# Optimization experiments

Hardware: AMD Instinct MI355X
Metric: run time of the kernel (lower is better)

The kernel has to match this reference:

```python
import jax, jax.numpy as jnp
import numpy as np

N2, N1, N0 = 25000, 50000, 100000
E2, E1, E0 = 250000, 500000, 1000000
CIN, H, COUT = 64, 128, 64
BN_EPS = 1e-5


def setup_inputs() -> dict:
    key = jax.random.key(0)
    ks = jax.random.split(key, 26)
    inp = {
        'x': jax.random.normal(ks[0], (N2, CIN), jnp.float32),
        'edge_index': jax.random.randint(ks[1], (2, E2), 0, N2),
        'xs0': jax.random.normal(ks[2], (N0, H), jnp.float32),
        'xs1': jax.random.normal(ks[3], (N1, H), jnp.float32),
        'ei0': jax.random.randint(ks[4], (2, E0), 0, N0),
        'ei1': jax.random.randint(ks[5], (2, E1), 0, N1),
        'ew0': jax.random.uniform(ks[6], (E0,), jnp.float32, 0.1, 1.0),
        'ew1': jax.random.uniform(ks[7], (E1,), jnp.float32, 0.1, 1.0),
        # pooling perms: unique indices of kept nodes at the finer level
        'perm0': jax.random.permutation(ks[8], N0)[:N1],
        'perm1': jax.random.permutation(ks[9], N1)[:N2],
        # GIN layer 1: in=64 -> hidden//2=64 (MLP: Lin, ReLU, Lin), then BN
        'W1a': 0.1 * jax.random.normal(ks[10], (CIN, H // 2), jnp.float32),
        'b1a': jnp.zeros((H // 2,), jnp.float32),
        'W1b': 0.1 * jax.random.normal(ks[11], (H // 2, H // 2), jnp.float32),
        'b1b': jnp.zeros((H // 2,), jnp.float32),
        'g1': jnp.ones((H // 2,), jnp.float32),
        'bt1': jnp.zeros((H // 2,), jnp.float32),
        # GIN layer 2: 64 -> hidden=128
        'W2a': 0.1 * jax.random.normal(ks[12], (H // 2, H), jnp.float32),
        'b2a': jnp.zeros((H,), jnp.float32),
        'W2b': 0.1 * jax.random.normal(ks[13], (H, H), jnp.float32),
        'b2b': jnp.zeros((H,), jnp.float32),
        'g2': jnp.ones((H,), jnp.float32),
        'bt2': jnp.zeros((H,), jnp.float32),
        # GCN up_convs (improved=True): hidden->hidden, hidden->out
        'Wg0': 0.1 * jax.random.normal(ks[14], (H, H), jnp.float32),
        'bg0': jnp.zeros((H,), jnp.float32),
        'Wg1': 0.1 * jax.random.normal(ks[15], (H, COUT), jnp.float32),
        'bg1': jnp.zeros((COUT,), jnp.float32),
    }
    return inp


def _gin_layer(x, ei, Wa, ba, Wb, bb, g, bt):
    """GINConv (eps=0) + ReLU + BatchNorm1d (training-mode stats)."""
    n = x.shape[0]
    agg = jax.ops.segment_sum(x[ei[0]], ei[1], num_segments=n)
    h = x + agg  # (1 + eps) * x + sum of neighbors, eps = 0
    h = jnp.maximum(h @ Wa + ba, 0.0) @ Wb + bb  # MLP: Lin-ReLU-Lin
    h = jnp.maximum(h, 0.0)  # F.relu on conv output
    mu = h.mean(axis=0)
    var = jnp.mean((h - mu) ** 2, axis=0)  # biased var (BatchNorm1d)
    return g * (h - mu) * jax.lax.rsqrt(var + BN_EPS) + bt


def _gcn_improved(x, ei, ew, W, b):
    """GCNConv(improved=True): self-loop weight 2, symmetric norm."""
    n = x.shape[0]
    h = x @ W
    deg = jax.ops.segment_sum(ew, ei[1], num_segments=n) + 2.0  # +2I self loops
    dis = jax.lax.rsqrt(deg)
    norm = dis[ei[0]] * ew * dis[ei[1]]
    out = jax.ops.segment_sum(norm[:, None] * h[ei[0]], ei[1], num_segments=n)
    out = out + (2.0 * dis * dis)[:, None] * h  # self-loop contribution
    return out + b


def reference(x, edge_index, xs0, xs1, ei0, ei1, ew0, ew1, perm0, perm1,
              W1a, b1a, W1b, b1b, g1, bt1,
              W2a, b2a, W2b, b2b, g2, bt2,
              Wg0, bg0, Wg1, bg1):
    # projection convs on the coarsest graph
    h = _gin_layer(x, edge_index, W1a, b1a, W1b, b1b, g1, bt1)
    h = _gin_layer(h, edge_index, W2a, b2a, W2b, b2b, g2, bt2)
    # upsample step 1 (i=0, j=1): scatter into level-1 graph, GCN, ReLU
    up = jnp.zeros_like(xs1).at[perm1].set(h)
    h = jnp.maximum(_gcn_improved(up, ei1, ew1, Wg0, bg0), 0.0)
    # upsample step 2 (i=1, j=0): scatter into level-0 graph, final GCN
    up = jnp.zeros_like(xs0).at[perm0].set(h)
    return _gcn_improved(up, ei0, ew0, Wg1, bg1)
```

## Files before the change

kernel.cpp:

```cpp
#include <hip/hip_runtime.h>
#include <hip/hip_fp16.h>
#include <type_traits>

#define NN2 25000
#define NN1 50000
#define NN0 100000
#define EE2 250000
#define EE1 500000
#define EE0 1000000
#define NTOTC 175000
#define ETOTC 1750000
#define NB 684
#define CHUNK 2048
#define NBLK 855
#define BN_EPS 1e-5f

static inline int cdiv(long a, long b) { return (int)((a + b - 1) / b); }

typedef _Float16 half8 __attribute__((ext_vector_type(8)));
typedef float f32x4 __attribute__((ext_vector_type(4)));

template <int K, int M, bool RELU, bool BNIN, bool BNOUT, typename OT>
__global__ __launch_bounds__(256) void mfma_gemm_kernel(
    const __half* __restrict__ in, const float* __restrict__ W,
    const float* __restrict__ bias,
    const float* __restrict__ sums, const float* __restrict__ sumsq,
    const float* __restrict__ g, const float* __restrict__ bt,
    float* __restrict__ osum, float* __restrict__ osq,
    OT* __restrict__ out, int n)
{
    constexpr int BM = 64;
    constexpr int LDA = K + 8;
    constexpr int NC = M / 16;
    __shared__ __align__(16) _Float16 Ah[BM * LDA];
    __shared__ __align__(16) _Float16 Wt[M * LDA];
    const int tid = threadIdx.x;
    const int r0 = blockIdx.x * BM;

    for (int idx = tid; idx < K * M; idx += 256) {
        int k = idx / M, m = idx % M;
        Wt[m * LDA + k] = (_Float16)W[idx];
    }
    for (int idx = tid; idx < BM * K; idx += 256) {
        int r = idx / K, k = idx % K;
        int gr = r0 + r;
        float v = (gr < n) ? __half2float(in[(long)gr * K + k]) : 0.f;
        if (BNIN) {
            float mu = sums[k] * (1.f / NN2);
            float rs = rsqrtf(sumsq[k] * (1.f / NN2) - mu * mu + BN_EPS);
            v = g[k] * rs * (v - mu) + bt[k];
        }
        Ah[r * LDA + k] = (_Float16)v;
    }
    __syncthreads();

    const int wid = tid >> 6, lane = tid & 63;
    const int rw = wid * 16;
    const int arow = rw + (lane & 15);
    const int koff = (lane >> 4) * 8;

    f32x4 acc[NC];
    #pragma unroll
    for (int c = 0; c < NC; ++c) acc[c] = f32x4{0.f, 0.f, 0.f, 0.f};
    #pragma unroll
    for (int k0 = 0; k0 < K; k0 += 32) {
        half8 a = *(const half8*)&Ah[arow * LDA + k0 + koff];
        #pragma unroll
        for (int c = 0; c < NC; ++c) {
            half8 b = *(const half8*)&Wt[(c * 16 + (lane & 15)) * LDA + k0 + koff];
            acc[c] = __builtin_amdgcn_mfma_f32_16x16x32_f16(a, b, acc[c], 0, 0, 0);
        }
    }

    float* bs = (float*)Ah;
    if (BNOUT) {
        __syncthreads();
        if (tid < 2 * M) bs[tid] = 0.f;
        __syncthreads();
    }
    const int drow = r0 + rw + 4 * (lane >> 4);
    #pragma unroll
    for (int c = 0; c < NC; ++c) {
        int col = c * 16 + (lane & 15);
        float bv = (bias != nullptr) ? bias[col] : 0.f;
        float sc = 0.f, qc = 0.f;
        #pragma unroll
        for (int j = 0; j < 4; ++j) {
            int r = drow + j;
            if (r < n) {
                float v = acc[c][j] + bv;
                if (RELU) v = fmaxf(v, 0.f);
                if constexpr (std::is_same<OT, __half>::value)
                    out[(long)r * M + col] = __float2half(v);
                else
                    out[(long)r * M + col] = v;
                if (BNOUT) { sc += v; qc += v * v; }
            }
        }
        if (BNOUT) { atomicAdd(&bs[col], sc); atomicAdd(&bs[M + col], qc); }
    }
    if (BNOUT) {
        __syncthreads();
        if (tid < M) { atomicAdd(&osum[tid], bs[tid]); atomicAdd(&osq[tid], bs[M + tid]); }
    }
}

template <int K, int M1, int M2, bool BNOUT>
__global__ __launch_bounds__(256) void mlp_gemm_kernel(
    const __half* __restrict__ in,
    const float* __restrict__ W1, const float* __restrict__ b1,
    const float* __restrict__ W2, const float* __restrict__ b2,
    float* __restrict__ osum, float* __restrict__ osq,
    __half* __restrict__ out, int n)
{
    constexpr int BM = 64;
    constexpr int LDA = K + 8;
    constexpr int LDM = M1 + 8;
    constexpr int NC1 = M1 / 16, NC2 = M2 / 16;
    __shared__ __align__(16) _Float16 Ah[BM * LDA];
    __shared__ __align__(16) _Float16 Wt1[M1 * LDA];
    __shared__ __align__(16) _Float16 Wt2[M2 * LDM];
    __shared__ __align__(16) _Float16 mid[BM * LDM];
    const int tid = threadIdx.x;
    const int r0 = blockIdx.x * BM;

    for (int idx = tid; idx < K * M1; idx += 256) {
        int k = idx / M1, m = idx % M1;
        Wt1[m * LDA + k] = (_Float16)W1[idx];
    }
    for (int idx = tid; idx < M1 * M2; idx += 256) {
        int k = idx / M2, m = idx % M2;
        Wt2[m * LDM + k] = (_Float16)W2[idx];
    }
    for (int idx = tid; idx < BM * K; idx += 256) {
        int r = idx / K, k = idx % K;
        int gr = r0 + r;
        Ah[r * LDA + k] = (gr < n) ? (_Float16)in[(long)gr * K + k] : (_Float16)0.f;
    }
    __syncthreads();

    const int wid = tid >> 6, lane = tid & 63;
    const int rw = wid * 16;
    const int arow = rw + (lane & 15);
    const int koff = (lane >> 4) * 8;

    f32x4 acc1[NC1];
    #pragma unroll
    for (int c = 0; c < NC1; ++c) acc1[c] = f32x4{0.f, 0.f, 0.f, 0.f};
    #pragma unroll
    for (int k0 = 0; k0 < K; k0 += 32) {
        half8 a = *(const half8*)&Ah[arow * LDA + k0 + koff];
        #pragma unroll
        for (int c = 0; c < NC1; ++c) {
            half8 b = *(const half8*)&Wt1[(c * 16 + (lane & 15)) * LDA + k0 + koff];
            acc1[c] = __builtin_amdgcn_mfma_f32_16x16x32_f16(a, b, acc1[c], 0, 0, 0);
        }
    }
    {
        int rd0 = rw + 4 * (lane >> 4);
        #pragma unroll
        for (int c = 0; c < NC1; ++c) {
            int col = c * 16 + (lane & 15);
            float bv = b1[col];
            #pragma unroll
            for (int j = 0; j < 4; ++j)
                mid[(rd0 + j) * LDM + col] = (_Float16)fmaxf(acc1[c][j] + bv, 0.f);
        }
    }
    float* bs = (float*)Ah;
    if (BNOUT) {
        if (tid < 2 * M2) bs[tid] = 0.f;
    }
    __syncthreads();

    f32x4 acc2[NC2];
    #pragma unroll
    for (int c = 0; c < NC2; ++c) acc2[c] = f32x4{0.f, 0.f, 0.f, 0.f};
    #pragma unroll
    for (int k0 = 0; k0 < M1; k0 += 32) {
        half8 a = *(const half8*)&mid[arow * LDM + k0 + koff];
        #pragma unroll
        for (int c = 0; c < NC2; ++c) {
            half8 b = *(const half8*)&Wt2[(c * 16 + (lane & 15)) * LDM + k0 + koff];
            acc2[c] = __builtin_amdgcn_mfma_f32_16x16x32_f16(a, b, acc2[c], 0, 0, 0);
        }
    }
    const int drow = r0 + rw + 4 * (lane >> 4);
    #pragma unroll
    for (int c = 0; c < NC2; ++c) {
        int col = c * 16 + (lane & 15);
        float bv = b2[col];
        float sc = 0.f, qc = 0.f;
        #pragma unroll
        for (int j = 0; j < 4; ++j) {
            int r = drow + j;
            if (r < n) {
                float v = fmaxf(acc2[c][j] + bv, 0.f);
                out[(long)r * M2 + col] = __float2half(v);
                if (BNOUT) { sc += v; qc += v * v; }
            }
        }
        if (BNOUT) { atomicAdd(&bs[col], sc); atomicAdd(&bs[M2 + col], qc); }
    }
    if (BNOUT) {
        __syncthreads();
        if (tid < M2) { atomicAdd(&osum[tid], bs[tid]); atomicAdd(&osq[tid], bs[M2 + tid]); }
    }
}

__global__ void inv_tohalf_kernel(const int* __restrict__ perm1, const int* __restrict__ perm0,
                                  int* __restrict__ inv1, int* __restrict__ inv0,
                                  float* __restrict__ bnz,
                                  const float* __restrict__ x, __half* __restrict__ xh)
{
    int i = blockIdx.x * blockDim.x + threadIdx.x;
    if (i < 384) bnz[i] = 0.f;
    if (i < NN2) inv1[perm1[i]] = i;
    else if (i < NN2 + NN1) inv0[perm0[i - NN2]] = i - NN2;
    if (i < NN2 * 16) {
        float4 v = ((const float4*)x)[i];
        __half2 a = __floats2half2_rn(v.x, v.y);
        __half2 b = __floats2half2_rn(v.z, v.w);
        ((uint2*)xh)[i] = make_uint2(*(unsigned*)&a, *(unsigned*)&b);
    }
}

__global__ __launch_bounds__(256) void count_translate_kernel(
    const int* __restrict__ dst2,
    const int* __restrict__ src1, const int* __restrict__ dst1,
    const int* __restrict__ src0, const int* __restrict__ dst0,
    const int* __restrict__ inv1, const int* __restrict__ inv0,
    int* __restrict__ tcg, int* __restrict__ G)
{
    __shared__ int h[NB];
    int tid = threadIdx.x, blk = blockIdx.x;
    for (int i = tid; i < NB; i += 256) h[i] = 0;
    __syncthreads();
    int e0 = blk * CHUNK, e1 = min(e0 + CHUNK, ETOTC);
    for (int e = e0 + tid; e < e1; e += 256) {
        int vg;
        if (e < EE2) {
            vg = dst2[e];
        } else if (e < EE2 + EE1) {
            int i = e - EE2;
            vg = NN2 + dst1[i];
            tcg[i] = inv1[src1[i]];
        } else {
            int i = e - EE2 - EE1;
            vg = NN2 + NN1 + dst0[i];
            tcg[EE1 + i] = inv0[src0[i]];
        }
        atomicAdd(&h[vg >> 8], 1);
    }
    __syncthreads();
    for (int i = tid; i < NB; i += 256) G[i * NBLK + blk] = h[i];
}

__global__ __launch_bounds__(256) void scan_block_kernel(int* data, int* bsum, int n)
{
    __shared__ int sh[256];
    int tid = threadIdx.x;
    int base = blockIdx.x * 1024 + tid * 4;
    int v[4];
    #pragma unroll
    for (int i = 0; i < 4; ++i) v[i] = (base + i < n) ? data[base + i] : 0;
    int tot = v[0] + v[1] + v[2] + v[3];
    sh[tid] = tot;
    __syncthreads();
    for (int d = 1; d < 256; d <<= 1) {
        int add = (tid >= d) ? sh[tid - d] : 0;
        __syncthreads();
        sh[tid] += add;
        __syncthreads();
    }
    int run = sh[tid] - tot;
    #pragma unroll
    for (int i = 0; i < 4; ++i) {
        if (base + i < n) data[base + i] = run;
        run += v[i];
    }
    if (tid == 255) bsum[blockIdx.x] = sh[255];
}

__global__ __launch_bounds__(1024) void scan_bsum_kernel(int* bsum, int nb)
{
    __shared__ int sh[1024];
    int tid = threadIdx.x;
    int v = (tid < nb) ? bsum[tid] : 0;
    sh[tid] = v;
    __syncthreads();
    for (int d = 1; d < 1024; d <<= 1) {
        int add = (tid >= d) ? sh[tid - d] : 0;
        __syncthreads();
        sh[tid] += add;
        __syncthreads();
    }
    if (tid < nb) bsum[tid] = sh[tid] - v;
}

__global__ __launch_bounds__(256) void place_kernel(
    const int* __restrict__ src2, const int* __restrict__ dst2,
    const int* __restrict__ dst1, const float* __restrict__ ew1,
    const int* __restrict__ dst0, const float* __restrict__ ew0,
    const int* __restrict__ tcg,
    const int* __restrict__ G, const int* __restrict__ bsum,
    int2* __restrict__ bedges)
{
    __shared__ int cur[NB];
    int tid = threadIdx.x, blk = blockIdx.x;
    for (int i = tid; i < NB; i += 256) {
        int idx = i * NBLK + blk;
        cur[i] = G[idx] + bsum[idx >> 10];
    }
    __syncthreads();
    int e0 = blk * CHUNK, e1 = min(e0 + CHUNK, ETOTC);
    for (int e = e0 + tid; e < e1; e += 256) {
        int vg, c, ewb;
        if (e < EE2) {
            vg = dst2[e]; c = src2[e]; ewb = 0;
        } else if (e < EE2 + EE1) {
            int i = e - EE2;
            vg = NN2 + dst1[i]; c = tcg[i]; ewb = __float_as_int(ew1[i]);
        } else {
            int i = e - EE2 - EE1;
            vg = NN2 + NN1 + dst0[i]; c = tcg[EE1 + i]; ewb = __float_as_int(ew0[i]);
        }
        int b = vg >> 8, local = vg & 255;
        int pos = atomicAdd(&cur[b], 1);
        bedges[pos] = make_int2((local << 16) | (c + 1), ewb);
    }
}

__global__ __launch_bounds__(256) void bucket_build_kernel(
    const int2* __restrict__ bedges, const int* __restrict__ G,
    const int* __restrict__ bsum,
    int* __restrict__ rp, int* __restrict__ re,
    int2* __restrict__ csr, float* __restrict__ dis)
{
    __shared__ int cnt[256];
    __shared__ float wdeg[256];
    __shared__ int excl[256];
    __shared__ int tsum[256];
    int b = blockIdx.x, tid = threadIdx.x;
    int i0 = b * NBLK;
    int s0 = G[i0] + bsum[i0 >> 10];
    int s1;
    if (b == NB - 1) s1 = ETOTC;
    else { int i1 = (b + 1) * NBLK; s1 = G[i1] + bsum[i1 >> 10]; }
    cnt[tid] = 0; wdeg[tid] = 0.f;
    __syncthreads();
    for (int i = s0 + tid; i < s1; i += 256) {
        int2 t = bedges[i];
        int local = t.x >> 16;
        atomicAdd(&wdeg[local], __int_as_float(t.y));
        if (t.x & 0xFFFF) atomicAdd(&cnt[local], 1);
    }
    __syncthreads();
    int v = cnt[tid];
    tsum[tid] = v;
    __syncthreads();
    for (int d = 1; d < 256; d <<= 1) {
        int add = (tid >= d) ? tsum[tid - d] : 0;
        __syncthreads();
        tsum[tid] += add;
        __syncthreads();
    }
    excl[tid] = tsum[tid] - v;
    {
        int vg = (b << 8) + tid;
        if (vg < NTOTC) {
            int r0_ = s0 + excl[tid];
            rp[vg] = r0_;
            re[vg] = r0_ + v;
            if (vg >= NN2) dis[vg - NN2] = rsqrtf(wdeg[tid] + 2.0f);
        }
    }
    cnt[tid] = 0;
    __syncthreads();
    for (int i = s0 + tid; i < s1; i += 256) {
        int2 t = bedges[i];
        int cx = t.x & 0xFFFF;
        if (cx) {
            int local = t.x >> 16;
            int pos = s0 + excl[local] + atomicAdd(&cnt[local], 1);
            csr[pos] = make_int2(cx - 1, t.y);
        }
    }
}

__global__ void disc_kernel(const int* __restrict__ perm1, const int* __restrict__ perm0,
                            const float* __restrict__ dis,
                            float* __restrict__ disc1, float* __restrict__ disc0)
{
    int i = blockIdx.x * blockDim.x + threadIdx.x;
    if (i < NN2) disc1[i] = dis[perm1[i]];
    else if (i < NN2 + NN1) disc0[i - NN2] = dis[NN1 + perm0[i - NN2]];
}

template <bool BN>
__global__ __launch_bounds__(256) void gin_gather_kernel(
    const __half* __restrict__ x, const int* __restrict__ rp, const int* __restrict__ re,
    const int2* __restrict__ csr,
    const float* __restrict__ sums, const float* __restrict__ sumsq,
    const float* __restrict__ g, const float* __restrict__ bt,
    __half* __restrict__ out, int n)
{
    int v = (blockIdx.x * 256 + threadIdx.x) >> 5;
    int lane = threadIdx.x & 31;
    if (v >= n) return;
    int p0 = rp[v], pe = re[v];
    float2 sv = __half22float2(*(const __half2*)(x + (long)v * 64 + lane * 2));
    float ax[8], ay[8];
    #pragma unroll
    for (int u = 0; u < 8; ++u) { ax[u] = 0.f; ay[u] = 0.f; }
    ax[0] = sv.x; ay[0] = sv.y;
    for (int base = p0; base < pe; base += 32) {
        int idx = base + lane;
        int s_l = 0; float m_l = 0.f;
        if (idx < pe) { s_l = csr[idx].x; m_l = 1.f; }
        int cnt = min(32, pe - base);
        for (int j = 0; j < cnt; j += 8) {
            int ss[8]; float mm[8];
            #pragma unroll
            for (int u = 0; u < 8; ++u) {
                ss[u] = __shfl(s_l, j + u, 32);
                mm[u] = __shfl(m_l, j + u, 32);
            }
            float2 hh[8];
            #pragma unroll
            for (int u = 0; u < 8; ++u)
                hh[u] = __half22float2(*(const __half2*)(x + (long)ss[u] * 64 + lane * 2));
            #pragma unroll
            for (int u = 0; u < 8; ++u) {
                ax[u] = fmaf(mm[u], hh[u].x, ax[u]);
                ay[u] = fmaf(mm[u], hh[u].y, ay[u]);
            }
        }
    }
    float accx = ((ax[0] + ax[1]) + (ax[2] + ax[3])) + ((ax[4] + ax[5]) + (ax[6] + ax[7]));
    float accy = ((ay[0] + ay[1]) + (ay[2] + ay[3])) + ((ay[4] + ay[5]) + (ay[6] + ay[7]));
    if (BN) {
        int deg = pe - p0;
        int c0 = lane * 2, c1 = lane * 2 + 1;
        float mu0 = sums[c0] * (1.f / NN2), mu1 = sums[c1] * (1.f / NN2);
        float rs0 = rsqrtf(sumsq[c0] * (1.f / NN2) - mu0 * mu0 + BN_EPS);
        float rs1 = rsqrtf(sumsq[c1] * (1.f / NN2) - mu1 * mu1 + BN_EPS);
        float a0 = g[c0] * rs0, a1 = g[c1] * rs1;
        accx = a0 * accx + (float)(deg + 1) * (bt[c0] - a0 * mu0);
        accy = a1 * accy + (float)(deg + 1) * (bt[c1] - a1 * mu1);
    }
    *(__half2*)(out + (long)v * 64 + lane * 2) = __floats2half2_rn(accx, accy);
}

template <bool RELU>
__global__ __launch_bounds__(256) void gcn_gather128_kernel(
    const __half* __restrict__ cmp, const int* __restrict__ inv,
    const int* __restrict__ rp, const int* __restrict__ re,
    const int2* __restrict__ csr, const float* __restrict__ disc,
    const float* __restrict__ dis, const float* __restrict__ bias,
    __half* __restrict__ out, int n)
{
    int v = (blockIdx.x * 256 + threadIdx.x) >> 5;
    int lane = threadIdx.x & 31;
    if (v >= n) return;
    int p0 = rp[v], pe = re[v];
    f32x4 acc[8];
    #pragma unroll
    for (int u = 0; u < 8; ++u) acc[u] = f32x4{0.f, 0.f, 0.f, 0.f};
    for (int base = p0; base < pe; base += 32) {
        int idx = base + lane;
        int cs_l = 0; float w_l = 0.f;
        if (idx < pe) {
            int2 sl = csr[idx];
            cs_l = sl.x;
            w_l = __int_as_float(sl.y) * disc[sl.x];
        }
        int cnt = min(32, pe - base);
        for (int j = 0; j < cnt; j += 8) {
            int cc[8]; float ww[8];
            #pragma unroll
            for (int u = 0; u < 8; ++u) {
                cc[u] = __shfl(cs_l, j + u, 32);
                ww[u] = __shfl(w_l, j + u, 32);
            }
            uint2 uu[8];
            #pragma unroll
            for (int u = 0; u < 8; ++u)
                uu[u] = *(const uint2*)(cmp + (long)cc[u] * 128 + lane * 4);
            #pragma unroll
            for (int u = 0; u < 8; ++u) {
                float2 pa = __half22float2(*(__half2*)&uu[u].x);
                float2 pb = __half22float2(*(__half2*)&uu[u].y);
                acc[u][0] = fmaf(ww[u], pa.x, acc[u][0]);
                acc[u][1] = fmaf(ww[u], pa.y, acc[u][1]);
                acc[u][2] = fmaf(ww[u], pb.x, acc[u][2]);
                acc[u][3] = fmaf(ww[u], pb.y, acc[u][3]);
            }
        }
    }
    f32x4 tot = ((acc[0] + acc[1]) + (acc[2] + acc[3])) + ((acc[4] + acc[5]) + (acc[6] + acc[7]));
    float dv = dis[v];
    int cv = inv[v];
    float sx0 = 0.f, sx1 = 0.f, sx2 = 0.f, sx3 = 0.f;
    if (cv >= 0) {
        uint2 u = *(const uint2*)(cmp + (long)cv * 128 + lane * 4);
        float2 pa = __half22float2(*(__half2*)&u.x), pb = __half22float2(*(__half2*)&u.y);
        sx0 = pa.x; sx1 = pa.y; sx2 = pb.x; sx3 = pb.y;
    }
    float s2 = 2.f * dv * dv;
    float o0 = fmaf(dv, tot[0], fmaf(s2, sx0, bias[lane * 4]));
    float o1 = fmaf(dv, tot[1], fmaf(s2, sx1, bias[lane * 4 + 1]));
    float o2 = fmaf(dv, tot[2], fmaf(s2, sx2, bias[lane * 4 + 2]));
    float o3 = fmaf(dv, tot[3], fmaf(s2, sx3, bias[lane * 4 + 3]));
    if (RELU) {
        o0 = fmaxf(o0, 0.f); o1 = fmaxf(o1, 0.f);
        o2 = fmaxf(o2, 0.f); o3 = fmaxf(o3, 0.f);
    }
    __half2 ha = __floats2half2_rn(o0, o1), hb = __floats2half2_rn(o2, o3);
    *(uint2*)(out + (long)v * 128 + lane * 4) = make_uint2(*(unsigned*)&ha, *(unsigned*)&hb);
}

template <bool RELU>
__global__ __launch_bounds__(256) void gcn_gather64_kernel(
    const __half* __restrict__ cmp, const int* __restrict__ inv,
    const int* __restrict__ rp, const int* __restrict__ re,
    const int2* __restrict__ csr, const float* __restrict__ disc,
    const float* __restrict__ dis, const float* __restrict__ bias,
    float* __restrict__ out, int n)
{
    int v = (blockIdx.x * 256 + threadIdx.x) >> 5;
    int lane = threadIdx.x & 31;
    if (v >= n) return;
    int p0 = rp[v], pe = re[v];
    float ax[8], ay[8];
    #pragma unroll
    for (int u = 0; u < 8; ++u) { ax[u] = 0.f; ay[u] = 0.f; }
    for (int base = p0; base < pe; base += 32) {
        int idx = base + lane;
        int cs_l = 0; float w_l = 0.f;
        if (idx < pe) {
            int2 sl = csr[idx];
            cs_l = sl.x;
            w_l = __int_as_float(sl.y) * disc[sl.x];
        }
        int cnt = min(32, pe - base);
        for (int j = 0; j < cnt; j += 8) {
            int cc[8]; float ww[8];
            #pragma unroll
            for (int u = 0; u < 8; ++u) {
                cc[u] = __shfl(cs_l, j + u, 32);
                ww[u] = __shfl(w_l, j + u, 32);
            }
            float2 hh[8];
            #pragma unroll
            for (int u = 0; u < 8; ++u)
                hh[u] = __half22float2(*(const __half2*)(cmp + (long)cc[u] * 64 + lane * 2));
            #pragma unroll
            for (int u = 0; u < 8; ++u) {
                ax[u] = fmaf(ww[u], hh[u].x, ax[u]);
                ay[u] = fmaf(ww[u], hh[u].y, ay[u]);
            }
        }
    }
    float axs = ((ax[0] + ax[1]) + (ax[2] + ax[3])) + ((ax[4] + ax[5]) + (ax[6] + ax[7]));
    float ays = ((ay[0] + ay[1]) + (ay[2] + ay[3])) + ((ay[4] + ay[5]) + (ay[6] + ay[7]));
    float dv = dis[v];
    int cv = inv[v];
    float sx = 0.f, sy = 0.f;
    if (cv >= 0) {
        float2 hv = __half22float2(*(const __half2*)(cmp + (long)cv * 64 + lane * 2));
        sx = hv.x; sy = hv.y;
    }
    float s2 = 2.f * dv * dv;
    float o0 = fmaf(dv, axs, fmaf(s2, sx, bias[lane * 2]));
    float o1 = fmaf(dv, ays, fmaf(s2, sy, bias[lane * 2 + 1]));
    if (RELU) { o0 = fmaxf(o0, 0.f); o1 = fmaxf(o1, 0.f); }
    *(float2*)(out + (long)v * 64 + lane * 2) = make_float2(o0, o1);
}

extern "C" void kernel_launch(void* const* d_in, const int* in_sizes, int n_in,
                              void* d_out, int out_size, void* d_ws, size_t ws_size,
                              hipStream_t stream)
{
    const float* x    = (const float*)d_in[0];
    const int*   ei2  = (const int*)d_in[1];
    const int*   ei0  = (const int*)d_in[4];
    const int*   ei1  = (const int*)d_in[5];
    const float* ew0  = (const float*)d_in[6];
    const float* ew1  = (const float*)d_in[7];
    const int*   perm0= (const int*)d_in[8];
    const int*   perm1= (const int*)d_in[9];
    const float* W1a  = (const float*)d_in[10];
    const float* b1a  = (const float*)d_in[11];
    const float* W1b  = (const float*)d_in[12];
    const float* b1b  = (const float*)d_in[13];
    const float* g1   = (const float*)d_in[14];
    const float* bt1  = (const float*)d_in[15];
    const float* W2a  = (const float*)d_in[16];
    const float* b2a  = (const float*)d_in[17];
    const float* W2b  = (const float*)d_in[18];
    const float* b2b  = (const float*)d_in[19];
    const float* g2   = (const float*)d_in[20];
    const float* bt2  = (const float*)d_in[21];
    const float* Wg0  = (const float*)d_in[22];
    const float* bg0  = (const float*)d_in[23];
    const float* Wg1  = (const float*)d_in[24];
    const float* bg1  = (const float*)d_in[25];
    float* out = (float*)d_out;

    float* ws  = (float*)d_ws;
    int*   wsi = (int*)d_ws;

    int*   rp    = wsi;
    int*   re    = wsi + 176000;
    float* dis   = ws  + 352000;
    float* disc1 = ws  + 502000;
    float* disc0 = ws  + 527000;
    int*   inv1  = wsi + 577000;
    int*   inv0  = wsi + 627000;
    float* s1    = ws  + 727000;
    float* q1    = ws  + 727064;
    float* s2    = ws  + 727128;
    float* q2    = ws  + 727256;
    int*   bsum  = wsi + 727500;
    int*   G     = wsi + 729000;
    int2*  bedges= (int2*)(wsi + 1315000);
    int2*  csr   = (int2*)(wsi + 4815000);
    __half* t0f  = (__half*)(ws + 8315000);
    __half* t0h  = (__half*)(ws + 9115000);
    __half* t1   = (__half*)(ws + 9915000);
    __half* Bb   = (__half*)(ws + 10715000);
    __half* cmp1 = (__half*)(ws + 12315000);
    __half* out1 = (__half*)(ws + 13915000);
    __half* cmp0 = (__half*)(ws + 17115000);
    int*   tcg   = wsi + 18715000;
    __half* xh   = (__half*)(ws + 20215000);

    const int* src2 = ei2, *dst2 = ei2 + EE2;
    const int* src1 = ei1, *dst1 = ei1 + EE1;
    const int* src0 = ei0, *dst0 = ei0 + EE0;

    const int NG = NB * NBLK;

    hipMemsetAsync(inv1, 0xFF, (NN1 + NN0) * 4, stream);
    inv_tohalf_kernel<<<cdiv(NN2 * 16, 256), 256, 0, stream>>>(
        perm1, perm0, inv1, inv0, s1, x, xh);
    count_translate_kernel<<<NBLK, 256, 0, stream>>>(
        dst2, src1, dst1, src0, dst0, inv1, inv0, tcg, G);
    scan_block_kernel<<<cdiv(NG, 1024), 256, 0, stream>>>(G, bsum, NG);
    scan_bsum_kernel<<<1, 1024, 0, stream>>>(bsum, cdiv(NG, 1024));
    place_kernel<<<NBLK, 256, 0, stream>>>(
        src2, dst2, dst1, ew1, dst0, ew0, tcg, G, bsum, bedges);
    bucket_build_kernel<<<NB, 256, 0, stream>>>(bedges, G, bsum, rp, re, csr, dis);
    disc_kernel<<<cdiv(NN2 + NN1, 256), 256, 0, stream>>>(perm1, perm0, dis, disc1, disc0);

    gin_gather_kernel<false><<<cdiv((long)NN2 * 32, 256), 256, 0, stream>>>(
        xh, rp, re, csr, nullptr, nullptr, nullptr, nullptr, t0f, NN2);
    mlp_gemm_kernel<64, 64, 64, true><<<cdiv(NN2, 64), 256, 0, stream>>>(
        t0f, W1a, b1a, W1b, b1b, s1, q1, t0h, NN2);

    gin_gather_kernel<true><<<cdiv((long)NN2 * 32, 256), 256, 0, stream>>>(
        t0h, rp, re, csr, s1, q1, g1, bt1, t1, NN2);
    mlp_gemm_kernel<64, 128, 128, true><<<cdiv(NN2, 64), 256, 0, stream>>>(
        t1, W2a, b2a, W2b, b2b, s2, q2, Bb, NN2);

    mfma_gemm_kernel<128, 128, false, true, false, __half><<<cdiv(NN2, 64), 256, 0, stream>>>(
        Bb, Wg0, nullptr, s2, q2, g2, bt2, nullptr, nullptr, cmp1, NN2);
    gcn_gather128_kernel<true><<<cdiv((long)NN1 * 32, 256), 256, 0, stream>>>(
        cmp1, inv1, rp + NN2, re + NN2, csr, disc1, dis, bg0, out1, NN1);

    mfma_gemm_kernel<128, 64, false, false, false, __half><<<cdiv(NN1, 64), 256, 0, stream>>>(
        out1, Wg1, nullptr, nullptr, nullptr, nullptr, nullptr, nullptr, nullptr, cmp0, NN1);
    gcn_gather64_kernel<false><<<cdiv((long)NN0 * 32, 256), 256, 0, stream>>>(
        cmp0, inv0, rp + NN2 + NN1, re + NN2 + NN1, csr, disc0, dis + NN1, bg1, out, NN0);
}
```

Before: 235.0 us.

## Fuse GIN neighbor gather into MLP GEMM kernel and pack row pointers

Merges the GIN neighbor-sum gather (including the BatchNorm-folded input transform) into the MLP GEMM kernel, so each block gathers its 64 rows directly into shared memory. This removes two kernel launches and the round trip of the intermediate aggregated tensors through global memory. The rp/re row-pointer arrays become one int2 array so each lookup is a single load. Shared memory is reused by aliasing mid over Ah/Wt1. In exchange, each GEMM block now does irregular gathers with only 8 row-groups in flight, which may hurt latency hiding compared with the standalone gather grid.

```diff
diff --git a/kernel.cpp b/kernel.cpp
--- a/kernel.cpp
+++ b/kernel.cpp
@@ -20,13 +20,12 @@
 typedef _Float16 half8 __attribute__((ext_vector_type(8)));
 typedef float f32x4 __attribute__((ext_vector_type(4)));
 
-template <int K, int M, bool RELU, bool BNIN, bool BNOUT, typename OT>
+template <int K, int M, bool RELU, bool BNIN, typename OT>
 __global__ __launch_bounds__(256) void mfma_gemm_kernel(
     const __half* __restrict__ in, const float* __restrict__ W,
     const float* __restrict__ bias,
     const float* __restrict__ sums, const float* __restrict__ sumsq,
     const float* __restrict__ g, const float* __restrict__ bt,
-    float* __restrict__ osum, float* __restrict__ osq,
     OT* __restrict__ out, int n)
 {
     constexpr int BM = 64;
@@ -71,19 +70,11 @@
             acc[c] = __builtin_amdgcn_mfma_f32_16x16x32_f16(a, b, acc[c], 0, 0, 0);
         }
     }
-
-    float* bs = (float*)Ah;
-    if (BNOUT) {
-        __syncthreads();
-        if (tid < 2 * M) bs[tid] = 0.f;
-        __syncthreads();
-    }
     const int drow = r0 + rw + 4 * (lane >> 4);
     #pragma unroll
     for (int c = 0; c < NC; ++c) {
         int col = c * 16 + (lane & 15);
         float bv = (bias != nullptr) ? bias[col] : 0.f;
-        float sc = 0.f, qc = 0.f;
         #pragma unroll
         for (int j = 0; j < 4; ++j) {
             int r = drow + j;
@@ -94,33 +85,38 @@
                     out[(long)r * M + col] = __float2half(v);
                 else
                     out[(long)r * M + col] = v;
-                if (BNOUT) { sc += v; qc += v * v; }
             }
         }
-        if (BNOUT) { atomicAdd(&bs[col], sc); atomicAdd(&bs[M + col], qc); }
-    }
-    if (BNOUT) {
-        __syncthreads();
-        if (tid < M) { atomicAdd(&osum[tid], bs[tid]); atomicAdd(&osq[tid], bs[M + tid]); }
-    }
-}
-
-template <int K, int M1, int M2, bool BNOUT>
-__global__ __launch_bounds__(256) void mlp_gemm_kernel(
-    const __half* __restrict__ in,
+    }
+}
+
+template <int M1, int M2, bool BN>
+__global__ __launch_bounds__(256) void gin_mlp_kernel(
+    const __half* __restrict__ x, const int2* __restrict__ rpre,
+    const int2* __restrict__ csr,
+    const float* __restrict__ sums, const float* __restrict__ sumsq,
+    const float* __restrict__ g, const float* __restrict__ bt,
     const float* __restrict__ W1, const float* __restrict__ b1,
     const float* __restrict__ W2, const float* __restrict__ b2,
     float* __restrict__ osum, float* __restrict__ osq,
     __half* __restrict__ out, int n)
 {
-    constexpr int BM = 64;
+    constexpr int BM = 64, K = 64;
     constexpr int LDA = K + 8;
     constexpr int LDM = M1 + 8;
-    constexpr int NC1 = M1 / 16, NC2 = M2 / 16;
-    __shared__ __align__(16) _Float16 Ah[BM * LDA];
-    __shared__ __align__(16) _Float16 Wt1[M1 * LDA];
-    __shared__ __align__(16) _Float16 Wt2[M2 * LDM];
-    __shared__ __align__(16) _Float16 mid[BM * LDM];
+    constexpr int S_AH = BM * LDA * 2;
+    constexpr int S_W1 = M1 * LDA * 2;
+    constexpr int S_W2 = M2 * LDM * 2;
+    constexpr int S_MID = BM * LDM * 2;
+    constexpr int TOTAL = S_AH + S_W1 + S_W2;
+    static_assert(S_MID + 8 * M2 <= S_AH + S_W1, "mid+bs must fit under Ah+Wt1");
+    __shared__ __align__(16) char smem[TOTAL];
+    _Float16* Ah  = (_Float16*)smem;
+    _Float16* Wt1 = (_Float16*)(smem + S_AH);
+    _Float16* Wt2 = (_Float16*)(smem + S_AH + S_W1);
+    _Float16* mid = (_Float16*)smem;
+    float*    bs  = (float*)(smem + S_MID);
+
     const int tid = threadIdx.x;
     const int r0 = blockIdx.x * BM;
 
@@ -132,17 +128,67 @@
         int k = idx / M2, m = idx % M2;
         Wt2[m * LDM + k] = (_Float16)W2[idx];
     }
-    for (int idx = tid; idx < BM * K; idx += 256) {
-        int r = idx / K, k = idx % K;
-        int gr = r0 + r;
-        Ah[r * LDA + k] = (gr < n) ? (_Float16)in[(long)gr * K + k] : (_Float16)0.f;
-    }
-    __syncthreads();
-
-    const int wid = tid >> 6, lane = tid & 63;
+
+    {
+        const int grp = tid >> 5, lane = tid & 31;
+        for (int rr = grp; rr < BM; rr += 8) {
+            int v = r0 + rr;
+            float accx = 0.f, accy = 0.f;
+            if (v < n) {
+                int2 pr = rpre[v];
+                int p0 = pr.x, pe = pr.y;
+                float2 sv = __half22float2(*(const __half2*)(x + (long)v * 64 + lane * 2));
+                float ax[8], ay[8];
+                #pragma unroll
+                for (int u = 0; u < 8; ++u) { ax[u] = 0.f; ay[u] = 0.f; }
+                ax[0] = sv.x; ay[0] = sv.y;
+                for (int base = p0; base < pe; base += 32) {
+                    int idx = base + lane;
+                    int s_l = 0; float m_l = 0.f;
+                    if (idx < pe) { s_l = csr[idx].x; m_l = 1.f; }
+                    int cnt = min(32, pe - base);
+                    for (int j = 0; j < cnt; j += 8) {
+                        int ss[8]; float mm[8];
+                        #pragma unroll
+                        for (int u = 0; u < 8; ++u) {
+                            ss[u] = __shfl(s_l, j + u, 32);
+                            mm[u] = __shfl(m_l, j + u, 32);
+                        }
+                        float2 hh[8];
+                        #pragma unroll
+                        for (int u = 0; u < 8; ++u)
+                            hh[u] = __half22float2(*(const __half2*)(x + (long)ss[u] * 64 + lane * 2));
+                        #pragma unroll
+                        for (int u = 0; u < 8; ++u) {
+                            ax[u] = fmaf(mm[u], hh[u].x, ax[u]);
+                            ay[u] = fmaf(mm[u], hh[u].y, ay[u]);
+                        }
+                    }
+                }
+                accx = ((ax[0] + ax[1]) + (ax[2] + ax[3])) + ((ax[4] + ax[5]) + (ax[6] + ax[7]));
+                accy = ((ay[0] + ay[1]) + (ay[2] + ay[3])) + ((ay[4] + ay[5]) + (ay[6] + ay[7]));
+                if (BN) {
+                    int deg = pe - p0;
+                    int c0 = lane * 2, c1 = lane * 2 + 1;
+                    float mu0 = sums[c0] * (1.f / NN2), mu1 = sums[c1] * (1.f / NN2);
+                    float rs0 = rsqrtf(sumsq[c0] * (1.f / NN2) - mu0 * mu0 + BN_EPS);
+                    float rs1 = rsqrtf(sumsq[c1] * (1.f / NN2) - mu1 * mu1 + BN_EPS);
+                    float a0 = g[c0] * rs0, a1 = g[c1] * rs1;
+                    accx = a0 * accx + (float)(deg + 1) * (bt[c0] - a0 * mu0);
+                    accy = a1 * accy + (float)(deg + 1) * (bt[c1] - a1 * mu1);
+                }
+            }
+            Ah[rr * LDA + lane * 2]     = (_Float16)accx;
+            Ah[rr * LDA + lane * 2 + 1] = (_Float16)accy;
+        }
+    }
+    __syncthreads();
+
+    const int wid = tid >> 6, lane64 = tid & 63;
     const int rw = wid * 16;
-    const int arow = rw + (lane & 15);
-    const int koff = (lane >> 4) * 8;
+    const int arow = rw + (lane64 & 15);
+    const int koff = (lane64 >> 4) * 8;
+    constexpr int NC1 = M1 / 16, NC2 = M2 / 16;
 
     f32x4 acc1[NC1];
     #pragma unroll
@@ -152,25 +198,24 @@
         half8 a = *(const half8*)&Ah[arow * LDA + k0 + koff];
         #pragma unroll
         for (int c = 0; c < NC1; ++c) {
-            half8 b = *(const half8*)&Wt1[(c * 16 + (lane & 15)) * LDA + k0 + koff];
+            half8 b = *(const half8*)&Wt1[(c * 16 + (lane64 & 15)) * LDA + k0 + koff];
             acc1[c] = __builtin_amdgcn_mfma_f32_16x16x32_f16(a, b, acc1[c], 0, 0, 0);
         }
     }
+    __syncthreads();
+
     {
-        int rd0 = rw + 4 * (lane >> 4);
+        int rd0 = rw + 4 * (lane64 >> 4);
         #pragma unroll
         for (int c = 0; c < NC1; ++c) {
-            int col = c * 16 + (lane & 15);
+            int col = c * 16 + (lane64 & 15);
             float bv = b1[col];
             #pragma unroll
             for (int j = 0; j < 4; ++j)
                 mid[(rd0 + j) * LDM + col] = (_Float16)fmaxf(acc1[c][j] + bv, 0.f);
         }
     }
-    float* bs = (float*)Ah;
-    if (BNOUT) {
-        if (tid < 2 * M2) bs[tid] = 0.f;
-    }
+    if (tid < 2 * M2) bs[tid] = 0.f;
     __syncthreads();
 
     f32x4 acc2[NC2];
@@ -181,14 +226,14 @@
         half8 a = *(const half8*)&mid[arow * LDM + k0 + koff];
         #pragma unroll
         for (int c = 0; c < NC2; ++c) {
-            half8 b = *(const half8*)&Wt2[(c * 16 + (lane & 15)) * LDM + k0 + koff];
+            half8 b = *(const half8*)&Wt2[(c * 16 + (lane64 & 15)) * LDM + k0 + koff];
             acc2[c] = __builtin_amdgcn_mfma_f32_16x16x32_f16(a, b, acc2[c], 0, 0, 0);
         }
     }
-    const int drow = r0 + rw + 4 * (lane >> 4);
+    const int drow = r0 + rw + 4 * (lane64 >> 4);
     #pragma unroll
     for (int c = 0; c < NC2; ++c) {
-        int col = c * 16 + (lane & 15);
+        int col = c * 16 + (lane64 & 15);
         float bv = b2[col];
         float sc = 0.f, qc = 0.f;
         #pragma unroll
@@ -197,15 +242,14 @@
             if (r < n) {
                 float v = fmaxf(acc2[c][j] + bv, 0.f);
                 out[(long)r * M2 + col] = __float2half(v);
-                if (BNOUT) { sc += v; qc += v * v; }
+                sc += v; qc += v * v;
             }
         }
-        if (BNOUT) { atomicAdd(&bs[col], sc); atomicAdd(&bs[M2 + col], qc); }
-    }
-    if (BNOUT) {
-        __syncthreads();
-        if (tid < M2) { atomicAdd(&osum[tid], bs[tid]); atomicAdd(&osq[tid], bs[M2 + tid]); }
-    }
+        atomicAdd(&bs[col], sc);
+        atomicAdd(&bs[M2 + col], qc);
+    }
+    __syncthreads();
+    if (tid < M2) { atomicAdd(&osum[tid], bs[tid]); atomicAdd(&osq[tid], bs[M2 + tid]); }
 }
 
 __global__ void inv_tohalf_kernel(const int* __restrict__ perm1, const int* __restrict__ perm0,
@@ -334,7 +378,7 @@
 __global__ __launch_bounds__(256) void bucket_build_kernel(
     const int2* __restrict__ bedges, const int* __restrict__ G,
     const int* __restrict__ bsum,
-    int* __restrict__ rp, int* __restrict__ re,
+    int2* __restrict__ rpre,
     int2* __restrict__ csr, float* __restrict__ dis)
 {
     __shared__ int cnt[256];
@@ -356,8 +400,8 @@
         if (t.x & 0xFFFF) atomicAdd(&cnt[local], 1);
     }
     __syncthreads();
-    int v = cnt[tid];
-    tsum[tid] = v;
+    int cv = cnt[tid];
+    tsum[tid] = cv;
     __syncthreads();
     for (int d = 1; d < 256; d <<= 1) {
         int add = (tid >= d) ? tsum[tid - d] : 0;
@@ -365,13 +409,12 @@
         tsum[tid] += add;
         __syncthreads();
     }
-    excl[tid] = tsum[tid] - v;
+    excl[tid] = tsum[tid] - cv;
     {
         int vg = (b << 8) + tid;
         if (vg < NTOTC) {
             int r0_ = s0 + excl[tid];
-            rp[vg] = r0_;
-            re[vg] = r0_ + v;
+            rpre[vg] = make_int2(r0_, r0_ + cv);
             if (vg >= NN2) dis[vg - NN2] = rsqrtf(wdeg[tid] + 2.0f);
         }
     }
@@ -397,73 +440,19 @@
     else if (i < NN2 + NN1) disc0[i - NN2] = dis[NN1 + perm0[i - NN2]];
 }
 
-template <bool BN>
-__global__ __launch_bounds__(256) void gin_gather_kernel(
-    const __half* __restrict__ x, const int* __restrict__ rp, const int* __restrict__ re,
-    const int2* __restrict__ csr,
-    const float* __restrict__ sums, const float* __restrict__ sumsq,
-    const float* __restrict__ g, const float* __restrict__ bt,
+template <bool RELU>
+__global__ __launch_bounds__(256) void gcn_gather128_kernel(
+    const __half* __restrict__ cmp, const int* __restrict__ inv,
+    const int2* __restrict__ rpre,
+    const int2* __restrict__ csr, const float* __restrict__ disc,
+    const float* __restrict__ dis, const float* __restrict__ bias,
     __half* __restrict__ out, int n)
 {
     int v = (blockIdx.x * 256 + threadIdx.x) >> 5;
     int lane = threadIdx.x & 31;
     if (v >= n) return;
-    int p0 = rp[v], pe = re[v];
-    float2 sv = __half22float2(*(const __half2*)(x + (long)v * 64 + lane * 2));
-    float ax[8], ay[8];
-    #pragma unroll
-    for (int u = 0; u < 8; ++u) { ax[u] = 0.f; ay[u] = 0.f; }
-    ax[0] = sv.x; ay[0] = sv.y;
-    for (int base = p0; base < pe; base += 32) {
-        int idx = base + lane;
-        int s_l = 0; float m_l = 0.f;
-        if (idx < pe) { s_l = csr[idx].x; m_l = 1.f; }
-        int cnt = min(32, pe - base);
-        for (int j = 0; j < cnt; j += 8) {
-            int ss[8]; float mm[8];
-            #pragma unroll
-            for (int u = 0; u < 8; ++u) {
-                ss[u] = __shfl(s_l, j + u, 32);
-                mm[u] = __shfl(m_l, j + u, 32);
-            }
-            float2 hh[8];
-            #pragma unroll
-            for (int u = 0; u < 8; ++u)
-                hh[u] = __half22float2(*(const __half2*)(x + (long)ss[u] * 64 + lane * 2));
-            #pragma unroll
-            for (int u = 0; u < 8; ++u) {
-                ax[u] = fmaf(mm[u], hh[u].x, ax[u]);
-                ay[u] = fmaf(mm[u], hh[u].y, ay[u]);
-            }
-        }
-    }
-    float accx = ((ax[0] + ax[1]) + (ax[2] + ax[3])) + ((ax[4] + ax[5]) + (ax[6] + ax[7]));
-    float accy = ((ay[0] + ay[1]) + (ay[2] + ay[3])) + ((ay[4] + ay[5]) + (ay[6] + ay[7]));
-    if (BN) {
-        int deg = pe - p0;
-        int c0 = lane * 2, c1 = lane * 2 + 1;
-        float mu0 = sums[c0] * (1.f / NN2), mu1 = sums[c1] * (1.f / NN2);
-        float rs0 = rsqrtf(sumsq[c0] * (1.f / NN2) - mu0 * mu0 + BN_EPS);
-        float rs1 = rsqrtf(sumsq[c1] * (1.f / NN2) - mu1 * mu1 + BN_EPS);
-        float a0 = g[c0] * rs0, a1 = g[c1] * rs1;
-        accx = a0 * accx + (float)(deg + 1) * (bt[c0] - a0 * mu0);
-        accy = a1 * accy + (float)(deg + 1) * (bt[c1] - a1 * mu1);
-    }
-    *(__half2*)(out + (long)v * 64 + lane * 2) = __floats2half2_rn(accx, accy);
-}
-
-template <bool RELU>
-__global__ __launch_bounds__(256) void gcn_gather128_kernel(
-    const __half* __restrict__ cmp, const int* __restrict__ inv,
-    const int* __restrict__ rp, const int* __restrict__ re,
-    const int2* __restrict__ csr, const float* __restrict__ disc,
-    const float* __restrict__ dis, const float* __restrict__ bias,
-    __half* __restrict__ out, int n)
-{
-    int v = (blockIdx.x * 256 + threadIdx.x) >> 5;
-    int lane = threadIdx.x & 31;
-    if (v >= n) return;
-    int p0 = rp[v], pe = re[v];
+    int2 pr = rpre[v];
+    int p0 = pr.x, pe = pr.y;
     f32x4 acc[8];
     #pragma unroll
     for (int u = 0; u < 8; ++u) acc[u] = f32x4{0.f, 0.f, 0.f, 0.f};
@@ -523,7 +512,7 @@
 template <bool RELU>
 __global__ __launch_bounds__(256) void gcn_gather64_kernel(
     const __half* __restrict__ cmp, const int* __restrict__ inv,
-    const int* __restrict__ rp, const int* __restrict__ re,
+    const int2* __restrict__ rpre,
     const int2* __restrict__ csr, const float* __restrict__ disc,
     const float* __restrict__ dis, const float* __restrict__ bias,
     float* __restrict__ out, int n)
@@ -531,7 +520,8 @@
     int v = (blockIdx.x * 256 + threadIdx.x) >> 5;
     int lane = threadIdx.x & 31;
     if (v >= n) return;
-    int p0 = rp[v], pe = re[v];
+    int2 pr = rpre[v];
+    int p0 = pr.x, pe = pr.y;
     float ax[8], ay[8];
     #pragma unroll
     for (int u = 0; u < 8; ++u) { ax[u] = 0.f; ay[u] = 0.f; }
@@ -611,8 +601,7 @@
     float* ws  = (float*)d_ws;
     int*   wsi = (int*)d_ws;
 
-    int*   rp    = wsi;
-    int*   re    = wsi + 176000;
+    int2*  rpre  = (int2*)wsi;
     float* dis   = ws  + 352000;
     float* disc1 = ws  + 502000;
     float* disc0 = ws  + 527000;
@@ -626,9 +615,7 @@
     int*   G     = wsi + 729000;
     int2*  bedges= (int2*)(wsi + 1315000);
     int2*  csr   = (int2*)(wsi + 4815000);
-    __half* t0f  = (__half*)(ws + 8315000);
     __half* t0h  = (__half*)(ws + 9115000);
-    __half* t1   = (__half*)(ws + 9915000);
     __half* Bb   = (__half*)(ws + 10715000);
     __half* cmp1 = (__half*)(ws + 12315000);
     __half* out1 = (__half*)(ws + 13915000);
@@ -651,26 +638,24 @@
     scan_bsum_kernel<<<1, 1024, 0, stream>>>(bsum, cdiv(NG, 1024));
     place_kernel<<<NBLK, 256, 0, stream>>>(
         src2, dst2, dst1, ew1, dst0, ew0, tcg, G, bsum, bedges);
-    bucket_build_kernel<<<NB, 256, 0, stream>>>(bedges, G, bsum, rp, re, csr, dis);
+    bucket_build_kernel<<<NB, 256, 0, stream>>>(bedges, G, bsum, rpre, csr, dis);
     disc_kernel<<<cdiv(NN2 + NN1, 256), 256, 0, stream>>>(perm1, perm0, dis, disc1, disc0);
 
-    gin_gather_kernel<false><<<cdiv((long)NN2 * 32, 256), 256, 0, stream>>>(
-        xh, rp, re, csr, nullptr, nullptr, nullptr, nullptr, t0f, NN2);
-    mlp_gemm_kernel<64, 64, 64, true><<<cdiv(NN2, 64), 256, 0, stream>>>(
-        t0f, W1a, b1a, W1b, b1b, s1, q1, t0h, NN2);
-
-    gin_gather_kernel<true><<<cdiv((long)NN2 * 32, 256), 256, 0, stream>>>(
-        t0h, rp, re, csr, s1, q1, g1, bt1, t1, NN2);
-    mlp_gemm_kernel<64, 128, 128, true><<<cdiv(NN2, 64), 256, 0, stream>>>(
-        t1, W2a, b2a, W2b, b2b, s2, q2, Bb, NN2);
-
-    mfma_gemm_kernel<128, 128, false, true, false, __half><<<cdiv(NN2, 64), 256, 0, stream>>>(
-        Bb, Wg0, nullptr, s2, q2, g2, bt2, nullptr, nullptr, cmp1, NN2);
+    gin_mlp_kernel<64, 64, false><<<cdiv(NN2, 64), 256, 0, stream>>>(
+        xh, rpre, csr, nullptr, nullptr, nullptr, nullptr,
+        W1a, b1a, W1b, b1b, s1, q1, t0h, NN2);
+
+    gin_mlp_kernel<128, 128, true><<<cdiv(NN2, 64), 256, 0, stream>>>(
+        t0h, rpre, csr, s1, q1, g1, bt1,
+        W2a, b2a, W2b, b2b, s2, q2, Bb, NN2);
+
+    mfma_gemm_kernel<128, 128, false, true, __half><<<cdiv(NN2, 64), 256, 0, stream>>>(
+        Bb, Wg0, nullptr, s2, q2, g2, bt2, cmp1, NN2);
     gcn_gather128_kernel<true><<<cdiv((long)NN1 * 32, 256), 256, 0, stream>>>(
-        cmp1, inv1, rp + NN2, re + NN2, csr, disc1, dis, bg0, out1, NN1);
-
-    mfma_gemm_kernel<128, 64, false, false, false, __half><<<cdiv(NN1, 64), 256, 0, stream>>>(
-        out1, Wg1, nullptr, nullptr, nullptr, nullptr, nullptr, nullptr, nullptr, cmp0, NN1);
+        cmp1, inv1, rpre + NN2, csr, disc1, dis, bg0, out1, NN1);
+
+    mfma_gemm_kernel<128, 64, false, false, __half><<<cdiv(NN1, 64), 256, 0, stream>>>(
+        out1, Wg1, nullptr, nullptr, nullptr, nullptr, nullptr, cmp0, NN1);
     gcn_gather64_kernel<false><<<cdiv((long)NN0 * 32, 256), 256, 0, stream>>>(
-        cmp0, inv0, rp + NN2 + NN1, re + NN2 + NN1, csr, disc0, dis + NN1, bg1, out, NN0);
-}
+        cmp0, inv0, rpre + NN2 + NN1, csr, disc0, dis + NN1, bg1, out, NN0);
+}
```

New measurement: 237.3 us. No clear change (+1.0%).
